# Kernel tuning notes

Measured on AMD Instinct MI355X. Metric: run time of the kernel, lower is better.

## Reference

```python
import jax, jax.numpy as jnp
import numpy as np

B, F, D, E, V1 = 16384, 26, 13, 16, 100001  # V1 = vocab + 1 (padding row 0)
H1, H2 = 128, 64
IN_DIM = F * E + D  # 429
EPS = 1e-5


def setup_inputs() -> dict:
    key = jax.random.key(0)
    ks = jax.random.split(key, 16)
    u = lambda k, shape, s=0.001: jax.random.uniform(k, shape, jnp.float32, -s, s)
    sparse_inputs = jax.random.randint(ks[0], (B, F), 0, V1, dtype=jnp.int32)
    dense_inputs = jax.random.normal(ks[1], (B, D), jnp.float32)
    emb_tables = u(ks[2], (F, V1, E)).at[:, 0, :].set(0.0)   # padding_idx=0 zeroed
    lin_tables = u(ks[3], (F, V1)).at[:, 0].set(0.0)
    lin_dense_w = u(ks[4], (D,))
    lin_dense_b = jnp.zeros((1,), jnp.float32)
    # BatchNorm (eval mode): gamma, beta, running_mean, running_var
    bn0 = (jnp.ones(IN_DIM), jnp.zeros(IN_DIM), 0.01 * jax.random.normal(ks[5], (IN_DIM,)), jnp.ones(IN_DIM))
    W1 = jax.random.normal(ks[6], (H1, IN_DIM)) * (1.0 / np.sqrt(IN_DIM))
    b1 = jnp.zeros(H1)
    bn1 = (jnp.ones(H1), jnp.zeros(H1), 0.01 * jax.random.normal(ks[7], (H1,)), jnp.ones(H1))
    W2 = jax.random.normal(ks[8], (H2, H1)) * (1.0 / np.sqrt(H1))
    b2 = jnp.zeros(H2)
    bn2 = (jnp.ones(H2), jnp.zeros(H2), 0.01 * jax.random.normal(ks[9], (H2,)), jnp.ones(H2))
    Wo = u(ks[10], (1, H2))
    bo = jnp.zeros(1)
    gbias = jnp.zeros(1)
    return dict(sparse_inputs=sparse_inputs, dense_inputs=dense_inputs,
                emb_tables=emb_tables, lin_tables=lin_tables,
                lin_dense_w=lin_dense_w, lin_dense_b=lin_dense_b,
                bn0_g=bn0[0], bn0_b=bn0[1], bn0_m=bn0[2], bn0_v=bn0[3],
                W1=W1, b1=b1, bn1_g=bn1[0], bn1_b=bn1[1], bn1_m=bn1[2], bn1_v=bn1[3],
                W2=W2, b2=b2, bn2_g=bn2[0], bn2_b=bn2[1], bn2_m=bn2[2], bn2_v=bn2[3],
                Wo=Wo, bo=bo, gbias=gbias)


def _bn(x, g, b, m, v):
    return (x - m) * jax.lax.rsqrt(v + EPS) * g + b


def reference(sparse_inputs, dense_inputs, emb_tables, lin_tables,
              lin_dense_w, lin_dense_b,
              bn0_g, bn0_b, bn0_m, bn0_v,
              W1, b1, bn1_g, bn1_b, bn1_m, bn1_v,
              W2, b2, bn2_g, bn2_b, bn2_m, bn2_v,
              Wo, bo, gbias):
    # gather per-feature embedding rows: [B, F, E] and linear terms [B, F]
    emb = jax.vmap(lambda tab, ix: tab[ix], in_axes=(0, 1), out_axes=1)(emb_tables, sparse_inputs)
    lin = jax.vmap(lambda tab, ix: tab[ix], in_axes=(0, 1), out_axes=1)(lin_tables, sparse_inputs)

    linear_sparse = jnp.sum(lin, axis=1, keepdims=True)                       # [B,1]
    linear_dense = dense_inputs @ lin_dense_w[:, None] + lin_dense_b          # [B,1]

    # FM: 0.5 * ((sum_f e)^2 - sum_f e^2), summed over embedding dim
    s = jnp.sum(emb, axis=1)
    fm = 0.5 * jnp.sum(s * s - jnp.sum(emb * emb, axis=1), axis=1, keepdims=True)  # [B,1]

    deep_in = jnp.concatenate([emb.reshape(emb.shape[0], -1), dense_inputs], axis=1)  # [B, F*E+D]
    h = _bn(deep_in, bn0_g, bn0_b, bn0_m, bn0_v)
    h = jax.nn.relu(_bn(h @ W1.T + b1, bn1_g, bn1_b, bn1_m, bn1_v))
    h = jax.nn.relu(_bn(h @ W2.T + b2, bn2_g, bn2_b, bn2_m, bn2_v))
    deep_out = h @ Wo.T + bo                                                   # [B,1]

    out = gbias + linear_sparse + linear_dense + fm + deep_out
    return out.squeeze(-1)
```

## Files before the change

### kernel.cpp

```cpp
#include <hip/hip_runtime.h>

#define BATCH  16384
#define NF     26
#define ND     13
#define NE     16
#define V1     100001
#define H1     128
#define H2     64
#define IN_DIM 429
#define KPAD   448
#define EPS    1e-5f

#define BM     32
#define SD     456
#define SH     136

typedef __attribute__((ext_vector_type(8))) short short8;
typedef __attribute__((ext_vector_type(4))) float f32x4;

static __device__ __forceinline__ unsigned short f2bf(float x) {
    unsigned int u = __float_as_uint(x);
    unsigned int r = (u + 0x7FFFu + ((u >> 16) & 1u)) >> 16;
    return (unsigned short)r;
}
static __device__ __forceinline__ float bf2f(unsigned short s) {
    return __uint_as_float(((unsigned int)s) << 16);
}

__global__ __launch_bounds__(256) void prep_kernel(
    const float* __restrict__ bn0_g, const float* __restrict__ bn0_b,
    const float* __restrict__ bn0_m, const float* __restrict__ bn0_v,
    const float* __restrict__ W1,    const float* __restrict__ b1,
    const float* __restrict__ bn1_g, const float* __restrict__ bn1_b,
    const float* __restrict__ bn1_m, const float* __restrict__ bn1_v,
    const float* __restrict__ W2,    const float* __restrict__ b2,
    const float* __restrict__ bn2_g, const float* __restrict__ bn2_b,
    const float* __restrict__ bn2_m, const float* __restrict__ bn2_v,
    const float* __restrict__ bo,    const float* __restrict__ gbias,
    const float* __restrict__ ldb,
    unsigned short* __restrict__ packB1, unsigned short* __restrict__ packB2,
    float* __restrict__ ceff, float* __restrict__ c2, float* __restrict__ constv)
{
    const int blk = blockIdx.x, tid = threadIdx.x;

    if (blk < 28) {
        int t    = blk * 256 + tid;
        int nblk = t / (14 * 64);
        int rem  = t % (14 * 64);
        int ks   = rem >> 6;
        int l    = rem & 63;
        int col  = nblk * 16 + (l & 15);
        float a1 = bn1_g[col] * rsqrtf(bn1_v[col] + EPS);
        int k0   = ks * 32 + ((l >> 4) << 3);
        union { short8 v; unsigned short u[8]; } tmp;
        #pragma unroll
        for (int j = 0; j < 8; ++j) {
            int k = k0 + j;
            float v = 0.f;
            if (k < IN_DIM) {
                float a0 = bn0_g[k] * rsqrtf(bn0_v[k] + EPS);
                v = W1[col * IN_DIM + k] * a0 * a1;
            }
            tmp.u[j] = f2bf(v);
        }
        *reinterpret_cast<short8*>(packB1 + (size_t)t * 8) = tmp.v;
    } else if (blk < 32) {
        int t    = (blk - 28) * 256 + tid;
        int nblk = t >> 8;
        int rem  = t & 255;
        int ks   = rem >> 6;
        int l    = rem & 63;
        int col  = nblk * 16 + (l & 15);
        float a2 = bn2_g[col] * rsqrtf(bn2_v[col] + EPS);
        int k0   = ks * 32 + ((l >> 4) << 3);
        union { short8 v; unsigned short u[8]; } tmp;
        #pragma unroll
        for (int j = 0; j < 8; ++j) {
            int k = k0 + j;
            tmp.u[j] = f2bf(W2[col * H1 + k] * a2);
        }
        *reinterpret_cast<short8*>(packB2 + (size_t)t * 8) = tmp.v;
    } else if (blk == 32) {
        int w = tid >> 6, l = tid & 63;
        for (int o = w; o < H1; o += 4) {
            float sum = 0.f;
            #pragma unroll
            for (int i = 0; i < 7; ++i) {
                int k = l + i * 64;
                if (k < IN_DIM) {
                    float a0 = bn0_g[k] * rsqrtf(bn0_v[k] + EPS);
                    float u0 = bn0_b[k] - a0 * bn0_m[k];
                    sum += u0 * W1[o * IN_DIM + k];
                }
            }
            sum += __shfl_xor(sum, 32);
            sum += __shfl_xor(sum, 16);
            sum += __shfl_xor(sum, 8);
            sum += __shfl_xor(sum, 4);
            sum += __shfl_xor(sum, 2);
            sum += __shfl_xor(sum, 1);
            if (l == 0) {
                float a1 = bn1_g[o] * rsqrtf(bn1_v[o] + EPS);
                ceff[o] = a1 * (sum + b1[o] - bn1_m[o]) + bn1_b[o];
            }
        }
    } else {
        if (tid < H2) {
            float a2 = bn2_g[tid] * rsqrtf(bn2_v[tid] + EPS);
            c2[tid] = a2 * (b2[tid] - bn2_m[tid]) + bn2_b[tid];
        } else if (tid == 64) {
            constv[0] = gbias[0] + bo[0] + ldb[0];
        }
    }
}

__global__ __launch_bounds__(256) void deepfm_main(
    const int*   __restrict__ sparse, const float* __restrict__ dense,
    const float* __restrict__ emb,    const float* __restrict__ lin,
    const float* __restrict__ ldw,
    const unsigned short* __restrict__ packB1,
    const unsigned short* __restrict__ packB2,
    const float* __restrict__ ceff, const float* __restrict__ c2w,
    const float* __restrict__ Wo,   const float* __restrict__ constv,
    float* __restrict__ out)
{
    __shared__ __align__(16) unsigned short deepS[BM][SD];
    __shared__ __align__(16) unsigned short h1S[BM][SH];
    __shared__ float accS[BM];

    const int tid = threadIdx.x;
    const int r0  = blockIdx.x * BM;

    if (tid < BM) accS[tid] = constv[0];
    for (int z = tid; z < BM * (KPAD - IN_DIM); z += 256) {
        int row = z / (KPAD - IN_DIM);
        int c   = IN_DIM + z % (KPAD - IN_DIM);
        deepS[row][c] = 0;
    }
    __syncthreads();

    #pragma unroll
    for (int it = 0; it < 13; ++it) {
        int q = tid + it * 256;
        int p = q >> 2, quarter = q & 3;
        int row = p / NF, f = p - row * NF;
        int idx = sparse[(r0 + row) * NF + f];
        const float* src = emb + ((size_t)f * V1 + (size_t)idx) * NE + quarter * 4;
        float4 v = *reinterpret_cast<const float4*>(src);
        ushort4 sv = { f2bf(v.x), f2bf(v.y), f2bf(v.z), f2bf(v.w) };
        *reinterpret_cast<ushort4*>(&deepS[row][f * NE + quarter * 4]) = sv;
        if (quarter == 0) {
            atomicAdd(&accS[row], lin[(size_t)f * V1 + (size_t)idx]);
        }
    }
    for (int t = tid; t < BM * ND; t += 256) {
        int row = t / ND, j = t - row * ND;
        float v = dense[(r0 + row) * ND + j];
        deepS[row][NF * NE + j] = f2bf(v);
        atomicAdd(&accS[row], v * ldw[j]);
    }
    __syncthreads();

    for (int t = tid; t < BM * NE; t += 256) {
        int row = t >> 4, e = t & 15;
        float s = 0.f, ss = 0.f;
        #pragma unroll
        for (int f = 0; f < NF; ++f) {
            float x = bf2f(deepS[row][f * NE + e]);
            s += x; ss += x * x;
        }
        atomicAdd(&accS[row], 0.5f * (s * s - ss));
    }

    const int w = tid >> 6, l = tid & 63;
    const int mblk = w & 1, nset = w >> 1;
    const int lr = l & 15, lq = l >> 4;

    f32x4 acc1[4] = { {0.f,0.f,0.f,0.f}, {0.f,0.f,0.f,0.f},
                      {0.f,0.f,0.f,0.f}, {0.f,0.f,0.f,0.f} };
    const short8* pB1 = reinterpret_cast<const short8*>(packB1);
    #pragma unroll
    for (int ks = 0; ks < KPAD / 32; ++ks) {
        short8 aF = *reinterpret_cast<const short8*>(&deepS[mblk * 16 + lr][ks * 32 + lq * 8]);
        #pragma unroll
        for (int nb = 0; nb < 4; ++nb) {
            int nblk = nset * 4 + nb;
            short8 bF = pB1[((size_t)nblk * 14 + ks) * 64 + l];
            acc1[nb] = __builtin_amdgcn_mfma_f32_16x16x32_bf16(aF, bF, acc1[nb], 0, 0, 0);
        }
    }
    #pragma unroll
    for (int nb = 0; nb < 4; ++nb) {
        int col = (nset * 4 + nb) * 16 + lr;
        float ce = ceff[col];
        #pragma unroll
        for (int r = 0; r < 4; ++r) {
            float h = fmaxf(acc1[nb][r] + ce, 0.f);
            h1S[mblk * 16 + lq * 4 + r][col] = f2bf(h);
        }
    }
    __syncthreads();

    f32x4 acc2[2] = { {0.f,0.f,0.f,0.f}, {0.f,0.f,0.f,0.f} };
    const short8* pB2 = reinterpret_cast<const short8*>(packB2);
    #pragma unroll
    for (int ks = 0; ks < 4; ++ks) {
        short8 aF = *reinterpret_cast<const short8*>(&h1S[mblk * 16 + lr][ks * 32 + lq * 8]);
        #pragma unroll
        for (int nb = 0; nb < 2; ++nb) {
            int nblk = nset * 2 + nb;
            short8 bF = pB2[((size_t)nblk * 4 + ks) * 64 + l];
            acc2[nb] = __builtin_amdgcn_mfma_f32_16x16x32_bf16(aF, bF, acc2[nb], 0, 0, 0);
        }
    }
    float part[4] = { 0.f, 0.f, 0.f, 0.f };
    #pragma unroll
    for (int nb = 0; nb < 2; ++nb) {
        int col = (nset * 2 + nb) * 16 + lr;
        float cv = c2w[col], wv = Wo[col];
        #pragma unroll
        for (int r = 0; r < 4; ++r) {
            float h = fmaxf(acc2[nb][r] + cv, 0.f);
            part[r] = fmaf(h, wv, part[r]);
        }
    }
    #pragma unroll
    for (int r = 0; r < 4; ++r) {
        part[r] += __shfl_xor(part[r], 1);
        part[r] += __shfl_xor(part[r], 2);
        part[r] += __shfl_xor(part[r], 4);
        part[r] += __shfl_xor(part[r], 8);
    }
    if (lr == 0) {
        #pragma unroll
        for (int r = 0; r < 4; ++r)
            atomicAdd(&accS[mblk * 16 + lq * 4 + r], part[r]);
    }
    __syncthreads();

    if (tid < BM) out[r0 + tid] = accS[tid];
}

extern "C" void kernel_launch(void* const* d_in, const int* in_sizes, int n_in,
                              void* d_out, int out_size, void* d_ws, size_t ws_size,
                              hipStream_t stream) {
    const int*   sparse = (const int*)d_in[0];
    const float* dense  = (const float*)d_in[1];
    const float* emb    = (const float*)d_in[2];
    const float* lin    = (const float*)d_in[3];
    const float* ldw    = (const float*)d_in[4];
    const float* ldb    = (const float*)d_in[5];
    const float* bn0g = (const float*)d_in[6],  *bn0b = (const float*)d_in[7];
    const float* bn0m = (const float*)d_in[8],  *bn0v = (const float*)d_in[9];
    const float* W1   = (const float*)d_in[10], *b1   = (const float*)d_in[11];
    const float* bn1g = (const float*)d_in[12], *bn1b = (const float*)d_in[13];
    const float* bn1m = (const float*)d_in[14], *bn1v = (const float*)d_in[15];
    const float* W2   = (const float*)d_in[16], *b2   = (const float*)d_in[17];
    const float* bn2g = (const float*)d_in[18], *bn2b = (const float*)d_in[19];
    const float* bn2m = (const float*)d_in[20], *bn2v = (const float*)d_in[21];
    const float* Wo   = (const float*)d_in[22], *bo   = (const float*)d_in[23];
    const float* gbias = (const float*)d_in[24];

    char* ws = (char*)d_ws;
    unsigned short* packB1 = (unsigned short*)ws;
    unsigned short* packB2 = (unsigned short*)(ws + 114688);
    float* ceff   = (float*)(ws + 131072);
    float* c2     = (float*)(ws + 131584);
    float* constv = (float*)(ws + 131840);

    prep_kernel<<<34, 256, 0, stream>>>(
        bn0g, bn0b, bn0m, bn0v, W1, b1, bn1g, bn1b, bn1m, bn1v,
        W2, b2, bn2g, bn2b, bn2m, bn2v, bo, gbias, ldb,
        packB1, packB2, ceff, c2, constv);

    deepfm_main<<<BATCH / BM, 256, 0, stream>>>(
        sparse, dense, emb, lin, ldw, packB1, packB2, ceff, c2, Wo, constv,
        (float*)d_out);
}
```

Baseline: 309.2 us.

## Use 512-thread blocks, stage sparse indices in LDS, split prep ceff across blocks

The main kernel moves from 256 to 512 threads per block. Each wave now owns one 16-column N block of layer 1 across both M halves, and one 16x16 tile of layer 2. Sparse indices are loaded into shared memory with vector loads before the gather, and the FM partials are reduced with shuffles before a single atomic per row. The ceff computation in the prep kernel is spread over eight blocks instead of one. The aim is more parallelism for latency hiding and a shorter serial prep tail, at the cost of each wave doing less MFMA work and issuing more B-fragment loads per block.

Result: faster. 272.5 us (-11.9%).

```diff
diff --git a/kernel.cpp b/kernel.cpp
--- a/kernel.cpp
+++ b/kernel.cpp
@@ -12,6 +12,7 @@
 #define EPS    1e-5f
 
 #define BM     32
+#define NT     512
 #define SD     456
 #define SH     136
 
@@ -80,13 +81,15 @@
             tmp.u[j] = f2bf(W2[col * H1 + k] * a2);
         }
         *reinterpret_cast<short8*>(packB2 + (size_t)t * 8) = tmp.v;
-    } else if (blk == 32) {
+    } else if (blk < 40) {
         int w = tid >> 6, l = tid & 63;
-        for (int o = w; o < H1; o += 4) {
+        #pragma unroll
+        for (int i = 0; i < 4; ++i) {
+            int o = (blk - 32) * 16 + w * 4 + i;
             float sum = 0.f;
             #pragma unroll
-            for (int i = 0; i < 7; ++i) {
-                int k = l + i * 64;
+            for (int it = 0; it < 7; ++it) {
+                int k = l + it * 64;
                 if (k < IN_DIM) {
                     float a0 = bn0_g[k] * rsqrtf(bn0_v[k] + EPS);
                     float u0 = bn0_b[k] - a0 * bn0_m[k];
@@ -114,7 +117,7 @@
     }
 }
 
-__global__ __launch_bounds__(256) void deepfm_main(
+__global__ __launch_bounds__(NT, 4) void deepfm_main(
     const int*   __restrict__ sparse, const float* __restrict__ dense,
     const float* __restrict__ emb,    const float* __restrict__ lin,
     const float* __restrict__ ldw,
@@ -126,115 +129,126 @@
 {
     __shared__ __align__(16) unsigned short deepS[BM][SD];
     __shared__ __align__(16) unsigned short h1S[BM][SH];
+    __shared__ __align__(16) int sparseS[BM * NF];
     __shared__ float accS[BM];
 
     const int tid = threadIdx.x;
     const int r0  = blockIdx.x * BM;
 
     if (tid < BM) accS[tid] = constv[0];
-    for (int z = tid; z < BM * (KPAD - IN_DIM); z += 256) {
-        int row = z / (KPAD - IN_DIM);
-        int c   = IN_DIM + z % (KPAD - IN_DIM);
-        deepS[row][c] = 0;
+    {
+        int z = tid;
+        if (z < BM * (KPAD - IN_DIM)) {
+            int row = z / (KPAD - IN_DIM), c = IN_DIM + z % (KPAD - IN_DIM);
+            deepS[row][c] = 0;
+        }
+        z = tid + NT;
+        if (z < BM * (KPAD - IN_DIM)) {
+            int row = z / (KPAD - IN_DIM), c = IN_DIM + z % (KPAD - IN_DIM);
+            deepS[row][c] = 0;
+        }
+    }
+    if (tid < BM * NF / 2) {
+        reinterpret_cast<int2*>(sparseS)[tid] =
+            reinterpret_cast<const int2*>(sparse + (size_t)r0 * NF)[tid];
     }
     __syncthreads();
 
     #pragma unroll
-    for (int it = 0; it < 13; ++it) {
-        int q = tid + it * 256;
-        int p = q >> 2, quarter = q & 3;
-        int row = p / NF, f = p - row * NF;
-        int idx = sparse[(r0 + row) * NF + f];
-        const float* src = emb + ((size_t)f * V1 + (size_t)idx) * NE + quarter * 4;
-        float4 v = *reinterpret_cast<const float4*>(src);
-        ushort4 sv = { f2bf(v.x), f2bf(v.y), f2bf(v.z), f2bf(v.w) };
-        *reinterpret_cast<ushort4*>(&deepS[row][f * NE + quarter * 4]) = sv;
-        if (quarter == 0) {
-            atomicAdd(&accS[row], lin[(size_t)f * V1 + (size_t)idx]);
-        }
-    }
-    for (int t = tid; t < BM * ND; t += 256) {
-        int row = t / ND, j = t - row * ND;
+    for (int it = 0; it < 7; ++it) {
+        int q = tid + it * NT;
+        if (q < BM * NF * 4) {
+            int p = q >> 2, quarter = q & 3;
+            int row = p / NF, f = p - row * NF;
+            int idx = sparseS[p];
+            const float* src = emb + ((size_t)f * V1 + (size_t)idx) * NE + quarter * 4;
+            float4 v = *reinterpret_cast<const float4*>(src);
+            ushort4 sv = { f2bf(v.x), f2bf(v.y), f2bf(v.z), f2bf(v.w) };
+            *reinterpret_cast<ushort4*>(&deepS[row][f * NE + quarter * 4]) = sv;
+            if (quarter == 0) {
+                atomicAdd(&accS[row], lin[(size_t)f * V1 + (size_t)idx]);
+            }
+        }
+    }
+    if (tid < BM * ND) {
+        int row = tid / ND, j = tid - row * ND;
         float v = dense[(r0 + row) * ND + j];
         deepS[row][NF * NE + j] = f2bf(v);
         atomicAdd(&accS[row], v * ldw[j]);
     }
     __syncthreads();
 
-    for (int t = tid; t < BM * NE; t += 256) {
-        int row = t >> 4, e = t & 15;
+    {
+        int row = tid >> 4, e = tid & 15;
         float s = 0.f, ss = 0.f;
         #pragma unroll
         for (int f = 0; f < NF; ++f) {
             float x = bf2f(deepS[row][f * NE + e]);
             s += x; ss += x * x;
         }
-        atomicAdd(&accS[row], 0.5f * (s * s - ss));
+        float fmv = 0.5f * (s * s - ss);
+        fmv += __shfl_xor(fmv, 1);
+        fmv += __shfl_xor(fmv, 2);
+        fmv += __shfl_xor(fmv, 4);
+        fmv += __shfl_xor(fmv, 8);
+        if (e == 0) atomicAdd(&accS[row], fmv);
     }
 
     const int w = tid >> 6, l = tid & 63;
-    const int mblk = w & 1, nset = w >> 1;
     const int lr = l & 15, lq = l >> 4;
 
-    f32x4 acc1[4] = { {0.f,0.f,0.f,0.f}, {0.f,0.f,0.f,0.f},
-                      {0.f,0.f,0.f,0.f}, {0.f,0.f,0.f,0.f} };
+    f32x4 acc1[2] = { {0.f,0.f,0.f,0.f}, {0.f,0.f,0.f,0.f} };
     const short8* pB1 = reinterpret_cast<const short8*>(packB1);
     #pragma unroll
     for (int ks = 0; ks < KPAD / 32; ++ks) {
-        short8 aF = *reinterpret_cast<const short8*>(&deepS[mblk * 16 + lr][ks * 32 + lq * 8]);
-        #pragma unroll
-        for (int nb = 0; nb < 4; ++nb) {
-            int nblk = nset * 4 + nb;
-            short8 bF = pB1[((size_t)nblk * 14 + ks) * 64 + l];
-            acc1[nb] = __builtin_amdgcn_mfma_f32_16x16x32_bf16(aF, bF, acc1[nb], 0, 0, 0);
-        }
-    }
-    #pragma unroll
-    for (int nb = 0; nb < 4; ++nb) {
-        int col = (nset * 4 + nb) * 16 + lr;
+        short8 aF0 = *reinterpret_cast<const short8*>(&deepS[lr     ][ks * 32 + lq * 8]);
+        short8 aF1 = *reinterpret_cast<const short8*>(&deepS[16 + lr][ks * 32 + lq * 8]);
+        short8 bF  = pB1[((size_t)w * 14 + ks) * 64 + l];
+        acc1[0] = __builtin_amdgcn_mfma_f32_16x16x32_bf16(aF0, bF, acc1[0], 0, 0, 0);
+        acc1[1] = __builtin_amdgcn_mfma_f32_16x16x32_bf16(aF1, bF, acc1[1], 0, 0, 0);
+    }
+    {
+        int col = w * 16 + lr;
         float ce = ceff[col];
         #pragma unroll
-        for (int r = 0; r < 4; ++r) {
-            float h = fmaxf(acc1[nb][r] + ce, 0.f);
-            h1S[mblk * 16 + lq * 4 + r][col] = f2bf(h);
-        }
-    }
-    __syncthreads();
-
-    f32x4 acc2[2] = { {0.f,0.f,0.f,0.f}, {0.f,0.f,0.f,0.f} };
+        for (int mb = 0; mb < 2; ++mb) {
+            #pragma unroll
+            for (int r = 0; r < 4; ++r) {
+                float h = fmaxf(acc1[mb][r] + ce, 0.f);
+                h1S[mb * 16 + lq * 4 + r][col] = f2bf(h);
+            }
+        }
+    }
+    __syncthreads();
+
+    const int mblk2 = w >> 2, nb2 = w & 3;
+    f32x4 acc2 = { 0.f, 0.f, 0.f, 0.f };
     const short8* pB2 = reinterpret_cast<const short8*>(packB2);
     #pragma unroll
     for (int ks = 0; ks < 4; ++ks) {
-        short8 aF = *reinterpret_cast<const short8*>(&h1S[mblk * 16 + lr][ks * 32 + lq * 8]);
-        #pragma unroll
-        for (int nb = 0; nb < 2; ++nb) {
-            int nblk = nset * 2 + nb;
-            short8 bF = pB2[((size_t)nblk * 4 + ks) * 64 + l];
-            acc2[nb] = __builtin_amdgcn_mfma_f32_16x16x32_bf16(aF, bF, acc2[nb], 0, 0, 0);
-        }
-    }
-    float part[4] = { 0.f, 0.f, 0.f, 0.f };
-    #pragma unroll
-    for (int nb = 0; nb < 2; ++nb) {
-        int col = (nset * 2 + nb) * 16 + lr;
+        short8 aF = *reinterpret_cast<const short8*>(&h1S[mblk2 * 16 + lr][ks * 32 + lq * 8]);
+        short8 bF = pB2[((size_t)nb2 * 4 + ks) * 64 + l];
+        acc2 = __builtin_amdgcn_mfma_f32_16x16x32_bf16(aF, bF, acc2, 0, 0, 0);
+    }
+    {
+        int col = nb2 * 16 + lr;
         float cv = c2w[col], wv = Wo[col];
+        float part[4];
+        #pragma unroll
+        for (int r = 0; r < 4; ++r)
+            part[r] = fmaxf(acc2[r] + cv, 0.f) * wv;
         #pragma unroll
         for (int r = 0; r < 4; ++r) {
-            float h = fmaxf(acc2[nb][r] + cv, 0.f);
-            part[r] = fmaf(h, wv, part[r]);
-        }
-    }
-    #pragma unroll
-    for (int r = 0; r < 4; ++r) {
-        part[r] += __shfl_xor(part[r], 1);
-        part[r] += __shfl_xor(part[r], 2);
-        part[r] += __shfl_xor(part[r], 4);
-        part[r] += __shfl_xor(part[r], 8);
-    }
-    if (lr == 0) {
-        #pragma unroll
-        for (int r = 0; r < 4; ++r)
-            atomicAdd(&accS[mblk * 16 + lq * 4 + r], part[r]);
+            part[r] += __shfl_xor(part[r], 1);
+            part[r] += __shfl_xor(part[r], 2);
+            part[r] += __shfl_xor(part[r], 4);
+            part[r] += __shfl_xor(part[r], 8);
+        }
+        if (lr == 0) {
+            #pragma unroll
+            for (int r = 0; r < 4; ++r)
+                atomicAdd(&accS[mblk2 * 16 + lq * 4 + r], part[r]);
+        }
     }
     __syncthreads();
 
@@ -268,12 +282,12 @@
     float* c2     = (float*)(ws + 131584);
     float* constv = (float*)(ws + 131840);
 
-    prep_kernel<<<34, 256, 0, stream>>>(
+    prep_kernel<<<41, 256, 0, stream>>>(
         bn0g, bn0b, bn0m, bn0v, W1, b1, bn1g, bn1b, bn1m, bn1v,
         W2, b2, bn2g, bn2b, bn2m, bn2v, bo, gbias, ldb,
         packB1, packB2, ceff, c2, constv);
 
-    deepfm_main<<<BATCH / BM, 256, 0, stream>>>(
+    deepfm_main<<<BATCH / BM, NT, 0, stream>>>(
         sparse, dense, emb, lin, ldw, packB1, packB2, ceff, c2, Wo, constv,
         (float*)d_out);
 }
```
